# Kernel tuning notes

Measured on AMD Instinct MI355X. Metric: run time of the kernel, lower is better.

Reference implementation:

```python
import jax, jax.numpy as jnp
import numpy as np

HEADS = 4

def _layernorm(x, g, b, eps=1e-5):
    mu = x.mean(-1, keepdims=True)
    var = ((x - mu) ** 2).mean(-1, keepdims=True)
    return (x - mu) / jnp.sqrt(var + eps) * g + b

def _feature_map(data, proj, is_query, eps=1e-4):
    # FAVOR+ softmax kernel features. data: [B,H,S,dh], proj: [m,dh]
    dh = data.shape[-1]
    m = proj.shape[0]
    dn = dh ** -0.25
    ratio = m ** -0.5
    dash = jnp.einsum('bhsd,md->bhsm', data * dn, proj)
    diag = 0.5 * jnp.sum((data * dn) ** 2, axis=-1, keepdims=True)
    mx = jnp.max(dash, axis=-1, keepdims=True) if is_query else jnp.max(dash)
    return ratio * (jnp.exp(dash - diag - mx) + eps)

def _causal_linear_attention(q, k, v):
    # q,k: [B,H,S,m] kernel features; v: [B,H,S,dh]
    k_cum = jnp.cumsum(k, axis=2)                                  # [B,H,S,m]
    d_inv = 1.0 / jnp.einsum('bhsm,bhsm->bhs', q, k_cum)           # [B,H,S]
    ctx = jnp.cumsum(jnp.einsum('bhsm,bhsd->bhsmd', k, v), axis=2) # [B,H,S,m,dh]
    return jnp.einsum('bhsmd,bhsm,bhs->bhsd', ctx, q, d_inv)

def reference(x, pre_w, pre_b, ln1_g, ln1_b, wq, wk, wv, wo, bo, proj,
              ln2_g, ln2_b, ff_w1, ff_b1, ff_w2, ff_b2, tgt_w, tgt_b, rd_w, rd_b):
    # preproc: 1x1x1 conv3d + softplus
    xbn = jax.nn.softplus(jnp.einsum('bcthw,oc->bothw', x, pre_w)
                          + pre_b[None, :, None, None, None])
    B, D, T, H, W = xbn.shape
    tokens = xbn.reshape(B, -1, D)  # raw torch-style reshape, S = T*H*W
    S = tokens.shape[1]

    # Performer block (depth=1): prenorm attention + prenorm FF, residuals
    h = _layernorm(tokens, ln1_g, ln1_b)
    split = lambda t: t.reshape(B, S, HEADS, -1).transpose(0, 2, 1, 3)
    q, k, v = split(h @ wq), split(h @ wk), split(h @ wv)
    qp = _feature_map(q, proj, True)
    kp = _feature_map(k, proj, False)
    attn = _causal_linear_attention(qp, kp, v)
    attn = attn.transpose(0, 2, 1, 3).reshape(B, S, D)
    tokens = tokens + attn @ wo + bo
    h2 = _layernorm(tokens, ln2_g, ln2_b)
    tokens = tokens + jax.nn.gelu(h2 @ ff_w1 + ff_b1, approximate=False) @ ff_w2 + ff_b2

    # readout
    out = tokens.reshape(B, D, T, H, W).mean(axis=2)               # [B,D,H,W]
    out = jnp.concatenate([out, x[:, 2, 0][:, None]], axis=1)      # [B,D+1,H,W]
    out = jax.lax.conv_general_dilated(out, tgt_w, (1, 1), [(2, 2), (2, 2)],
                                       dimension_numbers=('NCHW', 'OIHW', 'NCHW'))
    out = out + tgt_b[None, :, None, None]
    out = out.mean(axis=(2, 3))                                    # global avg pool -> [B,1]
    return out @ rd_w.T + rd_b


def setup_inputs() -> dict:
    key = jax.random.key(0)
    ks = jax.random.split(key, 12)
    B, T, H, W = 2, 8, 48, 48
    D, DH, M, FF = 64, 16, 32, 256
    s = lambda k, shape, sc=1.0: jax.random.normal(k, shape, jnp.float32) * sc
    inv = 1.0 / np.sqrt(D)
    return {
        'x': s(ks[0], (B, 3, T, H, W)),
        'pre_w': s(ks[1], (D, 3), 1.0 / np.sqrt(3)),
        'pre_b': jnp.zeros((D,), jnp.float32),
        'ln1_g': jnp.ones((D,), jnp.float32), 'ln1_b': jnp.zeros((D,), jnp.float32),
        'wq': s(ks[2], (D, D), inv), 'wk': s(ks[3], (D, D), inv), 'wv': s(ks[4], (D, D), inv),
        'wo': s(ks[5], (D, D), inv), 'bo': jnp.zeros((D,), jnp.float32),
        'proj': s(ks[6], (M, DH)),
        'ln2_g': jnp.ones((D,), jnp.float32), 'ln2_b': jnp.zeros((D,), jnp.float32),
        'ff_w1': s(ks[7], (D, FF), inv), 'ff_b1': jnp.zeros((FF,), jnp.float32),
        'ff_w2': s(ks[8], (FF, D), 1.0 / np.sqrt(FF)), 'ff_b2': jnp.zeros((D,), jnp.float32),
        'tgt_w': s(ks[9], (1, D + 1, 5, 5), 1.0 / np.sqrt((D + 1) * 25)),
        'tgt_b': jnp.zeros((1,), jnp.float32),
        'rd_w': s(ks[10], (1, 1)), 'rd_b': jnp.zeros((1,), jnp.float32),
    }
```

## Files before the change

### kernel.cpp

```cpp
#include <hip/hip_runtime.h>
#include <hip/hip_bf16.h>
#include <math.h>

typedef __hip_bfloat16 bf16;
typedef __attribute__((ext_vector_type(8))) short short8;
typedef __attribute__((ext_vector_type(16))) float floatx16;

constexpr int B_   = 2;
constexpr int T_   = 8;
constexpr int HW   = 48 * 48;
constexpr int S_   = T_ * HW;
constexpr int D_   = 64;
constexpr int NH   = 4;
constexpr int DH   = 16;
constexpr int M_   = 32;
constexpr int BS   = B_ * S_;
constexpr int BSD  = BS * D_;
constexpr int BH   = B_ * NH;
constexpr int BHS  = BH * S_;
constexpr int BHSM = BHS * M_;
constexpr int CHUNK = 32;
constexpr int NC   = S_ / CHUNK;
constexpr int STATE = M_ * DH + M_;
constexpr float DN = 0.5f;
constexpr float RATIO = 0.17677669529663687f;

__device__ __forceinline__ unsigned short f2bf(float f) {
  bf16 h = __float2bfloat16(f);
  return *reinterpret_cast<unsigned short*>(&h);
}
__device__ __forceinline__ float bf2f(bf16 v) { return __bfloat162float(v); }

__global__ void k_preln(const float* __restrict__ x, const float* __restrict__ pw,
                        const float* __restrict__ pb, const float* __restrict__ g,
                        const float* __restrict__ bb,
                        float* __restrict__ tok, bf16* __restrict__ h) {
  int token = blockIdx.x * 4 + (threadIdx.x >> 6);
  int lane = threadIdx.x & 63;
  int f = token * 64 + lane;
  int b = f / (D_ * S_);
  int r = f % (D_ * S_);
  int d = r / S_;
  int pos = r % S_;
  const float* xb = x + b * 3 * S_ + pos;
  float a = xb[0] * pw[d * 3 + 0] + xb[S_] * pw[d * 3 + 1] + xb[2 * S_] * pw[d * 3 + 2]
          + pb[d];
  float t = fmaxf(a, 0.f) + log1pf(expf(-fabsf(a)));
  tok[f] = t;
  float s1 = t, s2 = t * t;
  for (int off = 32; off; off >>= 1) {
    s1 += __shfl_xor(s1, off);
    s2 += __shfl_xor(s2, off);
  }
  float mu = s1 * (1.f / 64.f);
  float var = s2 * (1.f / 64.f) - mu * mu;
  float rs = rsqrtf(var + 1e-5f);
  h[f] = __float2bfloat16((t - mu) * rs * g[lane] + bb[lane]);
}

__global__ void __launch_bounds__(192) k_qkv(const bf16* __restrict__ h,
                      const float* __restrict__ wq, const float* __restrict__ wk,
                      const float* __restrict__ wv,
                      bf16* __restrict__ q, bf16* __restrict__ k, bf16* __restrict__ v) {
  int tid = threadIdx.x;
  int w = tid >> 6;
  int L = tid & 63;
  int half = L >> 5;
  int n = L & 31;
  int tbase = blockIdx.x * 32;
  const float* wm = (w == 0) ? wq : (w == 1) ? wk : wv;
  bf16* outm = (w == 0) ? q : (w == 1) ? k : v;

  short8 a[4];
  {
    const bf16* hrow = h + (size_t)(tbase + n) * 64 + half * 8;
#pragma unroll
    for (int c = 0; c < 4; ++c) a[c] = *(const short8*)(hrow + c * 16);
  }
#pragma unroll
  for (int ct = 0; ct < 2; ++ct) {
    int col = ct * 32 + n;
    short8 bfrag[4];
#pragma unroll
    for (int c = 0; c < 4; ++c) {
#pragma unroll
      for (int j = 0; j < 8; ++j)
        bfrag[c][j] = (short)f2bf(wm[(c * 16 + half * 8 + j) * 64 + col]);
    }
    floatx16 acc;
#pragma unroll
    for (int i = 0; i < 16; ++i) acc[i] = 0.f;
    acc = __builtin_amdgcn_mfma_f32_32x32x16_bf16(a[0], bfrag[0], acc, 0, 0, 0);
    acc = __builtin_amdgcn_mfma_f32_32x32x16_bf16(a[1], bfrag[1], acc, 0, 0, 0);
    acc = __builtin_amdgcn_mfma_f32_32x32x16_bf16(a[2], bfrag[2], acc, 0, 0, 0);
    acc = __builtin_amdgcn_mfma_f32_32x32x16_bf16(a[3], bfrag[3], acc, 0, 0, 0);
    int head = col >> 4, di = col & 15;
#pragma unroll
    for (int r = 0; r < 16; ++r) {
      int row = (r & 3) + 8 * (r >> 2) + 4 * half;
      int token = tbase + row;
      int b = token / S_, s = token % S_;
      outm[((size_t)(b * NH + head) * S_ + s) * DH + di] = __float2bfloat16(acc[r]);
    }
  }
}

__global__ void __launch_bounds__(256) k_feat(const bf16* __restrict__ q,
                      const bf16* __restrict__ k, const float* __restrict__ proj,
                      bf16* __restrict__ qpb, float* __restrict__ kp,
                      float* __restrict__ diagk, float* __restrict__ part) {
  int tid = threadIdx.x;
  int w = tid >> 6;
  int L = tid & 63;
  int half = L >> 5;
  int n = L & 31;
  int rowbase = blockIdx.x * 128 + w * 32;

  short8 qs = *(const short8*)(q + (size_t)(rowbase + n) * 16 + half * 8);
  short8 ks = *(const short8*)(k + (size_t)(rowbase + n) * 16 + half * 8);
  short8 aq, ak, bp;
  float dq = 0.f, dk = 0.f;
#pragma unroll
  for (int j = 0; j < 8; ++j) {
    float qf = __uint_as_float(((unsigned)(unsigned short)qs[j]) << 16) * DN;
    float kf = __uint_as_float(((unsigned)(unsigned short)ks[j]) << 16) * DN;
    dq += qf * qf; dk += kf * kf;
    aq[j] = (short)f2bf(qf);
    ak[j] = (short)f2bf(kf);
    bp[j] = (short)f2bf(proj[n * 16 + half * 8 + j]);
  }
  dq += __shfl_xor(dq, 32);
  dk += __shfl_xor(dk, 32);
  dq *= 0.5f; dk *= 0.5f;

  floatx16 Pq, Pk;
#pragma unroll
  for (int i = 0; i < 16; ++i) { Pq[i] = 0.f; Pk[i] = 0.f; }
  Pq = __builtin_amdgcn_mfma_f32_32x32x16_bf16(aq, bp, Pq, 0, 0, 0);
  Pk = __builtin_amdgcn_mfma_f32_32x32x16_bf16(ak, bp, Pk, 0, 0, 0);

  float bmax = -3.4e38f;
#pragma unroll
  for (int r = 0; r < 16; ++r) {
    int i = (r & 3) + 8 * (r >> 2) + 4 * half;
    kp[(size_t)(rowbase + i) * 32 + n] = Pk[r];
    bmax = fmaxf(bmax, Pk[r]);
  }
  if (L < 32) diagk[rowbase + n] = dk;
  for (int off = 32; off; off >>= 1) bmax = fmaxf(bmax, __shfl_xor(bmax, off));
  if (L == 0) part[blockIdx.x * 4 + w] = bmax;

#pragma unroll
  for (int r = 0; r < 16; ++r) {
    int i = (r & 3) + 8 * (r >> 2) + 4 * half;
    float mx = Pq[r];
    for (int off = 16; off; off >>= 1) mx = fmaxf(mx, __shfl_xor(mx, off, 32));
    float dqi = __shfl(dq, i, 64);
    float val = RATIO * (expf(Pq[r] - dqi - mx) + 1e-4f);
    qpb[(size_t)(rowbase + i) * 32 + n] = __float2bfloat16(val);
  }
}

__global__ void k_maxred(const float* __restrict__ part, float* __restrict__ gmax) {
  float m = -3.4e38f;
  for (int i = threadIdx.x; i < BHS / 32; i += 256) m = fmaxf(m, part[i]);
  __shared__ float red[256];
  red[threadIdx.x] = m;
  __syncthreads();
  for (int s = 128; s; s >>= 1) {
    if (threadIdx.x < s) red[threadIdx.x] = fmaxf(red[threadIdx.x], red[threadIdx.x + s]);
    __syncthreads();
  }
  if (!threadIdx.x) gmax[0] = red[0];
}

__global__ void __launch_bounds__(256) k_csfin(const float* __restrict__ diagk,
                      const float* __restrict__ gmax, const bf16* __restrict__ v,
                      const float* __restrict__ kp, bf16* __restrict__ kpb,
                      float* __restrict__ ckv) {
  __shared__ __align__(16) float sKp[CHUNK * 32];
  __shared__ __align__(16) float sVc[CHUNK * 16];
  int blk = blockIdx.x;
  int bh = blk / NC, c = blk % NC;
  int tid = threadIdx.x;
  int base = bh * S_ + c * CHUNK;
  float gm = gmax[0];
  {
    int row = tid >> 3, m4 = tid & 7;
    float4 dash = *(const float4*)&kp[(size_t)(base + row) * 32 + m4 * 4];
    float dg = diagk[base + row] + gm;
    float4 fin;
    fin.x = RATIO * (expf(dash.x - dg) + 1e-4f);
    fin.y = RATIO * (expf(dash.y - dg) + 1e-4f);
    fin.z = RATIO * (expf(dash.z - dg) + 1e-4f);
    fin.w = RATIO * (expf(dash.w - dg) + 1e-4f);
    *(float4*)&sKp[row * 32 + m4 * 4] = fin;
    uint2 u;
    u.x = (unsigned)f2bf(fin.x) | ((unsigned)f2bf(fin.y) << 16);
    u.y = (unsigned)f2bf(fin.z) | ((unsigned)f2bf(fin.w) << 16);
    *(uint2*)&kpb[(size_t)(base + row) * 32 + m4 * 4] = u;
  }
  if (tid < 128) {
    int row = tid >> 2, c4 = tid & 3;
    const bf16* vr = v + (size_t)(base + row) * 16 + c4 * 4;
    sVc[row * 16 + c4 * 4 + 0] = bf2f(vr[0]);
    sVc[row * 16 + c4 * 4 + 1] = bf2f(vr[1]);
    sVc[row * 16 + c4 * 4 + 2] = bf2f(vr[2]);
    sVc[row * 16 + c4 * 4 + 3] = bf2f(vr[3]);
  }
  __syncthreads();
  int m0 = tid >> 4, d0 = tid & 15;
  int m1 = m0 + 16;
  float a0 = 0.f, a1 = 0.f, az0 = 0.f, az1 = 0.f;
  for (int t = 0; t < CHUNK; ++t) {
    float k0 = sKp[t * 32 + m0];
    float k1 = sKp[t * 32 + m1];
    float vv = sVc[t * 16 + d0];
    a0 += k0 * vv;
    a1 += k1 * vv;
    if (d0 == 0) { az0 += k0; az1 += k1; }
  }
  float* outp = ckv + (size_t)blk * STATE;
  outp[m0 * 16 + d0] = a0;
  outp[m1 * 16 + d0] = a1;
  if (d0 == 0) { outp[512 + m0] = az0; outp[512 + m1] = az1; }
}

__global__ void k_prefix(float* __restrict__ ckv) {
  int idx = blockIdx.x * 256 + threadIdx.x;
  int bh = idx / STATE, c = idx % STATE;
  float run = 0.f;
  for (int j0 = 0; j0 < NC; j0 += 16) {
    float tb[16];
#pragma unroll
    for (int jj = 0; jj < 16; ++jj) tb[jj] = ckv[((size_t)bh * NC + j0 + jj) * STATE + c];
#pragma unroll
    for (int jj = 0; jj < 16; ++jj) {
      ckv[((size_t)bh * NC + j0 + jj) * STATE + c] = run;
      run += tb[jj];
    }
  }
}

__global__ void __launch_bounds__(256) k_attn(const bf16* __restrict__ qpb,
                                              const bf16* __restrict__ kpb,
                                              const bf16* __restrict__ v,
                                              const float* __restrict__ ckv,
                                              bf16* __restrict__ attn) {
  __shared__ __align__(16) float sP[4][32 * 33 + 4];
  int tid = threadIdx.x;
  int w = tid >> 6;
  int L = tid & 63;
  int half = L >> 5;
  int n = L & 31;
  int chunk = blockIdx.x * 4 + w;
  int bh = chunk / NC, c = chunk % NC;
  int base = bh * S_ + c * CHUNK;

  short8 a1 = *(const short8*)(qpb + (size_t)(base + n) * 32 + half * 8);
  short8 a2 = *(const short8*)(qpb + (size_t)(base + n) * 32 + 16 + half * 8);
  short8 b1 = *(const short8*)(kpb + (size_t)(base + n) * 32 + half * 8);
  short8 b2 = *(const short8*)(kpb + (size_t)(base + n) * 32 + 16 + half * 8);

  floatx16 P;
#pragma unroll
  for (int i = 0; i < 16; ++i) P[i] = 0.f;
  P = __builtin_amdgcn_mfma_f32_32x32x16_bf16(a1, b1, P, 0, 0, 0);
  P = __builtin_amdgcn_mfma_f32_32x32x16_bf16(a2, b2, P, 0, 0, 0);

  float* sp = &sP[w][0];
#pragma unroll
  for (int r = 0; r < 16; ++r) {
    int i = (r & 3) + 8 * (r >> 2) + 4 * half;
    sp[i * 33 + n] = (n <= i) ? P[r] : 0.f;
  }
  __syncthreads();
  short8 pa1, pa2;
#pragma unroll
  for (int j = 0; j < 8; ++j) {
    pa1[j] = (short)f2bf(sp[n * 33 + half * 8 + j]);
    pa2[j] = (short)f2bf(sp[n * 33 + 16 + half * 8 + j]);
  }

  const float* cs = ckv + (size_t)chunk * STATE;
  const unsigned short one_bf = f2bf(1.f);
  short8 vb1, vb2, sb1, sb2;
#pragma unroll
  for (int j = 0; j < 8; ++j) {
    int t1 = half * 8 + j, t2 = 16 + half * 8 + j;
    vb1[j] = (n < 16) ? *(const short*)(v + (size_t)(base + t1) * 16 + n)
                      : (short)(n == 16 ? one_bf : 0);
    vb2[j] = (n < 16) ? *(const short*)(v + (size_t)(base + t2) * 16 + n)
                      : (short)(n == 16 ? one_bf : 0);
    float y1 = (n < 16) ? cs[t1 * 16 + n] : (n == 16 ? cs[512 + t1] : 0.f);
    float y2 = (n < 16) ? cs[t2 * 16 + n] : (n == 16 ? cs[512 + t2] : 0.f);
    sb1[j] = (short)f2bf(y1);
    sb2[j] = (short)f2bf(y2);
  }

  floatx16 O;
#pragma unroll
  for (int i = 0; i < 16; ++i) O[i] = 0.f;
  O = __builtin_amdgcn_mfma_f32_32x32x16_bf16(pa1, vb1, O, 0, 0, 0);
  O = __builtin_amdgcn_mfma_f32_32x32x16_bf16(pa2, vb2, O, 0, 0, 0);
  O = __builtin_amdgcn_mfma_f32_32x32x16_bf16(a1, sb1, O, 0, 0, 0);
  O = __builtin_amdgcn_mfma_f32_32x32x16_bf16(a2, sb2, O, 0, 0, 0);

  int srcl = 16 + 32 * half;
  float res[16];
#pragma unroll
  for (int r = 0; r < 16; ++r) {
    float den = __shfl(O[r], srcl, 64);
    res[r] = O[r] / den;
  }
  if (n < 16) {
    int b = bh >> 2, head = bh & 3;
#pragma unroll
    for (int r = 0; r < 16; ++r) {
      int i = (r & 3) + 8 * (r >> 2) + 4 * half;
      attn[((size_t)(b * S_ + c * CHUNK + i)) * 64 + head * 16 + n] = __float2bfloat16(res[r]);
    }
  }
}

__global__ void __launch_bounds__(128) k_wo_ln(const bf16* __restrict__ attn,
                        const float* __restrict__ wo, const float* __restrict__ bo,
                        const float* __restrict__ tok, const float* __restrict__ g,
                        const float* __restrict__ bb,
                        float* __restrict__ tok2, bf16* __restrict__ h2) {
  __shared__ __align__(16) float sC[32 * 68];
  int tid = threadIdx.x;
  int w = tid >> 6;
  int L = tid & 63;
  int half = L >> 5;
  int n = L & 31;
  int tbase = blockIdx.x * 32;

  short8 a[4];
  {
    const bf16* arow = attn + (size_t)(tbase + n) * 64 + half * 8;
#pragma unroll
    for (int c = 0; c < 4; ++c) a[c] = *(const short8*)(arow + c * 16);
  }
  int col = w * 32 + n;
  short8 bfrag[4];
#pragma unroll
  for (int c = 0; c < 4; ++c) {
#pragma unroll
    for (int j = 0; j < 8; ++j)
      bfrag[c][j] = (short)f2bf(wo[(c * 16 + half * 8 + j) * 64 + col]);
  }
  floatx16 acc;
#pragma unroll
  for (int i = 0; i < 16; ++i) acc[i] = 0.f;
  acc = __builtin_amdgcn_mfma_f32_32x32x16_bf16(a[0], bfrag[0], acc, 0, 0, 0);
  acc = __builtin_amdgcn_mfma_f32_32x32x16_bf16(a[1], bfrag[1], acc, 0, 0, 0);
  acc = __builtin_amdgcn_mfma_f32_32x32x16_bf16(a[2], bfrag[2], acc, 0, 0, 0);
  acc = __builtin_amdgcn_mfma_f32_32x32x16_bf16(a[3], bfrag[3], acc, 0, 0, 0);
  float bias = bo[col];
#pragma unroll
  for (int r = 0; r < 16; ++r) {
    int row = (r & 3) + 8 * (r >> 2) + 4 * half;
    sC[row * 68 + col] = acc[r] + tok[(size_t)(tbase + row) * 64 + col] + bias;
  }
  __syncthreads();
  int tg = tid >> 5, cg = tid & 31;
  int c0 = cg * 2, c1 = c0 + 1;
  float g0 = g[c0], g1 = g[c1], be0 = bb[c0], be1 = bb[c1];
#pragma unroll
  for (int i = 0; i < 8; ++i) {
    int lrow = tg * 8 + i;
    int token = tbase + lrow;
    float t0 = sC[lrow * 68 + c0];
    float t1 = sC[lrow * 68 + c1];
    float s1 = t0 + t1, s2 = t0 * t0 + t1 * t1;
    for (int off = 16; off; off >>= 1) {
      s1 += __shfl_xor(s1, off, 32);
      s2 += __shfl_xor(s2, off, 32);
    }
    float mu = s1 * (1.f / 64.f);
    float var = s2 * (1.f / 64.f) - mu * mu;
    float rs = rsqrtf(var + 1e-5f);
    tok2[token * 64 + c0] = t0;
    tok2[token * 64 + c1] = t1;
    h2[token * 64 + c0] = __float2bfloat16((t0 - mu) * rs * g0 + be0);
    h2[token * 64 + c1] = __float2bfloat16((t1 - mu) * rs * g1 + be1);
  }
}

__global__ void __launch_bounds__(256) k_ffg(const bf16* __restrict__ h2,
                                             const float* __restrict__ w1,
                                             const float* __restrict__ b1,
                                             float* __restrict__ Gavg) {
  int tid = threadIdx.x;
  int w = tid >> 6;
  int L = tid & 63;
  int half = L >> 5;
  int n = L & 31;
  int blk = blockIdx.x;
  int b = blk / 576;
  int rem = blk % 576;
  int ch = rem / 9;
  int jp0 = (rem % 9) * 4;
  int token_n = b * 18432 + ch * 288 + (n & 7) * 36 + jp0 + (n >> 3);

  short8 a[4];
  {
    const bf16* hrow = h2 + (size_t)token_n * 64 + half * 8;
#pragma unroll
    for (int c = 0; c < 4; ++c) a[c] = *(const short8*)(hrow + c * 16);
  }
  size_t gbase = ((size_t)(b * 64 + ch) * 36 + jp0);
#pragma unroll
  for (int ct = 0; ct < 2; ++ct) {
    int col = w * 64 + ct * 32 + n;
    short8 bfrag[4];
#pragma unroll
    for (int c = 0; c < 4; ++c) {
#pragma unroll
      for (int j = 0; j < 8; ++j)
        bfrag[c][j] = (short)f2bf(w1[(c * 16 + half * 8 + j) * 256 + col]);
    }
    floatx16 acc;
#pragma unroll
    for (int i = 0; i < 16; ++i) acc[i] = 0.f;
    acc = __builtin_amdgcn_mfma_f32_32x32x16_bf16(a[0], bfrag[0], acc, 0, 0, 0);
    acc = __builtin_amdgcn_mfma_f32_32x32x16_bf16(a[1], bfrag[1], acc, 0, 0, 0);
    acc = __builtin_amdgcn_mfma_f32_32x32x16_bf16(a[2], bfrag[2], acc, 0, 0, 0);
    acc = __builtin_amdgcn_mfma_f32_32x32x16_bf16(a[3], bfrag[3], acc, 0, 0, 0);
    float bias = b1[col];
#pragma unroll
    for (int j = 0; j < 4; ++j) {
      float s = 0.f;
#pragma unroll
      for (int rr = 0; rr < 4; ++rr) {
        float xg = acc[j * 4 + rr] + bias;
        s += 0.5f * xg * (1.f + erff(xg * 0.70710678118654752f));
      }
      s += __shfl_xor(s, 32);
      if (half == 0)
        Gavg[(gbase + j) * 256 + col] = s * 0.125f;
    }
  }
}

__global__ void __launch_bounds__(256) k_pool2(const float* __restrict__ Gavg,
                        const float* __restrict__ tok2, const float* __restrict__ w2,
                        const float* __restrict__ b2, float* __restrict__ pool) {
  __shared__ __align__(16) float sG[18 * 256];
  __shared__ __align__(16) float sRed[4 * 18 * 64];
  int blk = blockIdx.x;
  int b = blk / 128;
  int rem = blk % 128;
  int ch = rem >> 1, jph = rem & 1;
  int tid = threadIdx.x;
  size_t grow0 = ((size_t)(b * 64 + ch) * 36 + jph * 18) * 256;
  for (int e = tid; e < 1152; e += 256) {
    int row = e >> 6, c4 = e & 63;
    *(float4*)&sG[row * 256 + c4 * 4] = *(const float4*)&Gavg[grow0 + row * 256 + c4 * 4];
  }
  __syncthreads();
  int kg = tid >> 6, dd = tid & 63;
  float acc[18];
#pragma unroll
  for (int i = 0; i < 18; ++i) acc[i] = 0.f;
  for (int k4 = 0; k4 < 16; ++k4) {
    int k = kg * 64 + k4 * 4;
    float w0 = w2[(k + 0) * 64 + dd];
    float w1 = w2[(k + 1) * 64 + dd];
    float w2v = w2[(k + 2) * 64 + dd];
    float w3 = w2[(k + 3) * 64 + dd];
#pragma unroll
    for (int i = 0; i < 18; ++i) {
      float4 gf = *(const float4*)&sG[i * 256 + k];
      acc[i] += gf.x * w0 + gf.y * w1 + gf.z * w2v + gf.w * w3;
    }
  }
#pragma unroll
  for (int i = 0; i < 18; ++i) sRed[(kg * 18 + i) * 64 + dd] = acc[i];
  __syncthreads();
  for (int o = tid; o < 1152; o += 256) {
    int jp18 = o >> 6, d2 = o & 63;
    float gsum = sRed[(0 * 18 + jp18) * 64 + d2] + sRed[(1 * 18 + jp18) * 64 + d2]
               + sRed[(2 * 18 + jp18) * 64 + d2] + sRed[(3 * 18 + jp18) * 64 + d2];
    int p = (jph * 18 + jp18) * 64 + d2;
    size_t tbase = (size_t)b * 1179648 + (size_t)ch * 18432 + p;
    float ts = 0.f;
#pragma unroll
    for (int t = 0; t < 8; ++t) ts += tok2[tbase + t * 2304];
    pool[((size_t)(b * 64 + ch)) * HW + p] = ts * 0.125f + gsum + b2[d2];
  }
}

__global__ void __launch_bounds__(256) k_convsum(const float* __restrict__ pool,
                                                 const float* __restrict__ x,
                                                 const float* __restrict__ w,
                                                 float* __restrict__ partial) {
  int blk = blockIdx.x;
  int b = blk / 65, ch = blk % 65;
  int tid = threadIdx.x;
  __shared__ float cls[25];
  __shared__ float red[256];
  if (tid < 25) {
    int ry = tid / 5, rx = tid % 5;
    int kh0 = (ry <= 2) ? 0 : (ry == 3 ? 1 : 2);
    int kh1 = (ry >= 2) ? 4 : (ry == 1 ? 3 : 2);
    int kw0 = (rx <= 2) ? 0 : (rx == 3 ? 1 : 2);
    int kw1 = (rx >= 2) ? 4 : (rx == 1 ? 3 : 2);
    float s = 0.f;
    for (int kh = kh0; kh <= kh1; ++kh)
      for (int kw = kw0; kw <= kw1; ++kw)
        s += w[ch * 25 + kh * 5 + kw];
    cls[tid] = s;
  }
  __syncthreads();
  const float* pc = (ch < 64) ? (pool + ((size_t)(b * 64 + ch)) * HW)
                              : (x + (size_t)b * 3 * S_ + 2 * S_);
  float acc = 0.f;
#pragma unroll
  for (int e = tid; e < HW; e += 256) {
    int iy = e / 48, ix = e % 48;
    int ry = (iy == 0) ? 0 : (iy == 1) ? 1 : (iy <= 45) ? 2 : (iy == 46) ? 3 : 4;
    int rx = (ix == 0) ? 0 : (ix == 1) ? 1 : (ix <= 45) ? 2 : (ix == 46) ? 3 : 4;
    acc += pc[e] * cls[ry * 5 + rx];
  }
  red[tid] = acc;
  __syncthreads();
  for (int s = 128; s; s >>= 1) {
    if (tid < s) red[tid] += red[tid + s];
    __syncthreads();
  }
  if (!tid) partial[blk] = red[0];
}

__global__ void k_final(const float* __restrict__ partial, const float* __restrict__ tgt_b,
                        const float* __restrict__ rd_w, const float* __restrict__ rd_b,
                        float* __restrict__ out) {
  int b = blockIdx.x;
  int lane = threadIdx.x;
  float s = (lane < 65) ? partial[b * 65 + lane] : 0.f;
  for (int off = 32; off; off >>= 1) s += __shfl_down(s, off, 64);
  __shared__ float r2;
  if (lane == 64) r2 = s;
  __syncthreads();
  if (!lane) {
    float tot = s + r2;
    float mean = tot / 2304.f + tgt_b[0];
    out[b] = mean * rd_w[0] + rd_b[0];
  }
}

extern "C" void kernel_launch(void* const* d_in, const int* in_sizes, int n_in,
                              void* d_out, int out_size, void* d_ws, size_t ws_size,
                              hipStream_t stream) {
  const float* x     = (const float*)d_in[0];
  const float* pre_w = (const float*)d_in[1];
  const float* pre_b = (const float*)d_in[2];
  const float* ln1_g = (const float*)d_in[3];
  const float* ln1_b = (const float*)d_in[4];
  const float* wq    = (const float*)d_in[5];
  const float* wk    = (const float*)d_in[6];
  const float* wv    = (const float*)d_in[7];
  const float* wo    = (const float*)d_in[8];
  const float* bo    = (const float*)d_in[9];
  const float* proj  = (const float*)d_in[10];
  const float* ln2_g = (const float*)d_in[11];
  const float* ln2_b = (const float*)d_in[12];
  const float* ff_w1 = (const float*)d_in[13];
  const float* ff_b1 = (const float*)d_in[14];
  const float* ff_w2 = (const float*)d_in[15];
  const float* ff_b2 = (const float*)d_in[16];
  const float* tgt_w = (const float*)d_in[17];
  const float* tgt_b = (const float*)d_in[18];
  const float* rd_w  = (const float*)d_in[19];
  const float* rd_b  = (const float*)d_in[20];
  float* out = (float*)d_out;

  float* ws = (float*)d_ws;
  float* tok   = ws;
  bf16*  v     = (bf16*)(ws + (size_t)BSD);
  bf16*  q     = (bf16*)(ws + 2 * (size_t)BSD);
  float* Gavg  = ws + 2 * (size_t)BSD;
  float* pool  = Gavg + 1179648;
  bf16*  k     = (bf16*)(ws + 3 * (size_t)BSD);
  bf16*  h     = (bf16*)(ws + 4 * (size_t)BSD);
  float* kp    = ws + 4 * (size_t)BSD;
  bf16*  qpb   = (bf16*)(ws + 6 * (size_t)BSD);
  bf16*  kpb   = (bf16*)(ws + 7 * (size_t)BSD);
  float* ckv   = ws + 8 * (size_t)BSD;
  float* tok2  = ws + 8 * (size_t)BSD;
  bf16*  attnb = k;
  bf16*  h2    = h;
  float* smalls = ws + 9 * (size_t)BSD + 147456;
  float* diagk = smalls;
  float* part  = diagk + BHS;
  float* gmax  = part + BHSM / 256;
  float* partial = gmax + 64;

  k_preln<<<dim3(BS / 4), dim3(256), 0, stream>>>(x, pre_w, pre_b, ln1_g, ln1_b, tok, h);
  k_qkv<<<dim3(BS / 32), dim3(192), 0, stream>>>(h, wq, wk, wv, q, k, v);
  k_feat<<<dim3(BHS / 128), dim3(256), 0, stream>>>(q, k, proj, qpb, kp, diagk, part);
  k_maxred<<<dim3(1), dim3(256), 0, stream>>>(part, gmax);
  k_csfin<<<dim3(BH * NC), dim3(256), 0, stream>>>(diagk, gmax, v, kp, kpb, ckv);
  k_prefix<<<dim3(BH * STATE / 256), dim3(256), 0, stream>>>(ckv);
  k_attn<<<dim3(BH * NC / 4), dim3(256), 0, stream>>>(qpb, kpb, v, ckv, attnb);
  k_wo_ln<<<dim3(BS / 32), dim3(128), 0, stream>>>(attnb, wo, bo, tok, ln2_g, ln2_b, tok2, h2);
  k_ffg<<<dim3(B_ * 64 * 9), dim3(256), 0, stream>>>(h2, ff_w1, ff_b1, Gavg);
  k_pool2<<<dim3(B_ * 64 * 2), dim3(256), 0, stream>>>(Gavg, tok2, ff_w2, ff_b2, pool);
  k_convsum<<<dim3(B_ * 65), dim3(256), 0, stream>>>(pool, x, tgt_w, partial);
  k_final<<<dim3(B_), dim3(128), 0, stream>>>(partial, tgt_b, rd_w, rd_b, out);
}
```

Measured before the change: 222.9 us.

## Split chunk-state prefix scan into three-phase segmented scan; store residual tokens as bf16

The single serial prefix-sum kernel over 576 chunks per head is replaced by a three-phase segmented scan: per-segment sums, a scan over the 18 segment sums, then a per-segment rescan seeded with its offset. This raises parallelism from BH*STATE threads to 18 times that, so the former long serial dependency chain is spread over many more waves. Separately, the residual token buffers tok and tok2 are stored as bf16 instead of fp32 to halve their memory traffic. The cost is two extra launches, an extra read of the chunk states, and reduced precision on the residual stream.

```diff
diff --git a/kernel.cpp b/kernel.cpp
--- a/kernel.cpp
+++ b/kernel.cpp
@@ -21,6 +21,8 @@
 constexpr int BHSM = BHS * M_;
 constexpr int CHUNK = 32;
 constexpr int NC   = S_ / CHUNK;
+constexpr int NSEG = 18;
+constexpr int SEGLEN = 32;
 constexpr int STATE = M_ * DH + M_;
 constexpr float DN = 0.5f;
 constexpr float RATIO = 0.17677669529663687f;
@@ -34,7 +36,7 @@
 __global__ void k_preln(const float* __restrict__ x, const float* __restrict__ pw,
                         const float* __restrict__ pb, const float* __restrict__ g,
                         const float* __restrict__ bb,
-                        float* __restrict__ tok, bf16* __restrict__ h) {
+                        bf16* __restrict__ tok, bf16* __restrict__ h) {
   int token = blockIdx.x * 4 + (threadIdx.x >> 6);
   int lane = threadIdx.x & 63;
   int f = token * 64 + lane;
@@ -46,7 +48,7 @@
   float a = xb[0] * pw[d * 3 + 0] + xb[S_] * pw[d * 3 + 1] + xb[2 * S_] * pw[d * 3 + 2]
           + pb[d];
   float t = fmaxf(a, 0.f) + log1pf(expf(-fabsf(a)));
-  tok[f] = t;
+  tok[f] = __float2bfloat16(t);
   float s1 = t, s2 = t * t;
   for (int off = 32; off; off >>= 1) {
     s1 += __shfl_xor(s1, off);
@@ -226,18 +228,51 @@
   if (d0 == 0) { outp[512 + m0] = az0; outp[512 + m1] = az1; }
 }
 
-__global__ void k_prefix(float* __restrict__ ckv) {
+__global__ void k_scan1(const float* __restrict__ ckv, float* __restrict__ segsum) {
   int idx = blockIdx.x * 256 + threadIdx.x;
-  int bh = idx / STATE, c = idx % STATE;
+  int c = idx % STATE;
+  int rem = idx / STATE;
+  int seg = rem % NSEG;
+  int bh = rem / NSEG;
+  size_t base = ((size_t)bh * NC + seg * SEGLEN) * STATE + c;
+  float s = 0.f;
+#pragma unroll 8
+  for (int i = 0; i < SEGLEN; ++i) s += ckv[base + (size_t)i * STATE];
+  segsum[idx] = s;
+}
+
+__global__ void k_scan2(float* __restrict__ segsum) {
+  int idx = blockIdx.x * 256 + threadIdx.x;
+  int c = idx % STATE;
+  int bh = idx / STATE;
+  float tb[NSEG];
+#pragma unroll
+  for (int s = 0; s < NSEG; ++s)
+    tb[s] = segsum[((size_t)bh * NSEG + s) * STATE + c];
   float run = 0.f;
-  for (int j0 = 0; j0 < NC; j0 += 16) {
-    float tb[16];
-#pragma unroll
-    for (int jj = 0; jj < 16; ++jj) tb[jj] = ckv[((size_t)bh * NC + j0 + jj) * STATE + c];
-#pragma unroll
-    for (int jj = 0; jj < 16; ++jj) {
-      ckv[((size_t)bh * NC + j0 + jj) * STATE + c] = run;
-      run += tb[jj];
+#pragma unroll
+  for (int s = 0; s < NSEG; ++s) {
+    segsum[((size_t)bh * NSEG + s) * STATE + c] = run;
+    run += tb[s];
+  }
+}
+
+__global__ void k_scan3(float* __restrict__ ckv, const float* __restrict__ segsum) {
+  int idx = blockIdx.x * 256 + threadIdx.x;
+  int c = idx % STATE;
+  int rem = idx / STATE;
+  int seg = rem % NSEG;
+  int bh = rem / NSEG;
+  float run = segsum[idx];
+  size_t base = ((size_t)bh * NC + seg * SEGLEN) * STATE + c;
+  for (int i0 = 0; i0 < SEGLEN; i0 += 8) {
+    float tb[8];
+#pragma unroll
+    for (int j = 0; j < 8; ++j) tb[j] = ckv[base + (size_t)(i0 + j) * STATE];
+#pragma unroll
+    for (int j = 0; j < 8; ++j) {
+      ckv[base + (size_t)(i0 + j) * STATE] = run;
+      run += tb[j];
     }
   }
 }
@@ -325,9 +360,9 @@
 
 __global__ void __launch_bounds__(128) k_wo_ln(const bf16* __restrict__ attn,
                         const float* __restrict__ wo, const float* __restrict__ bo,
-                        const float* __restrict__ tok, const float* __restrict__ g,
+                        const bf16* __restrict__ tok, const float* __restrict__ g,
                         const float* __restrict__ bb,
-                        float* __restrict__ tok2, bf16* __restrict__ h2) {
+                        bf16* __restrict__ tok2, bf16* __restrict__ h2) {
   __shared__ __align__(16) float sC[32 * 68];
   int tid = threadIdx.x;
   int w = tid >> 6;
@@ -361,7 +396,7 @@
 #pragma unroll
   for (int r = 0; r < 16; ++r) {
     int row = (r & 3) + 8 * (r >> 2) + 4 * half;
-    sC[row * 68 + col] = acc[r] + tok[(size_t)(tbase + row) * 64 + col] + bias;
+    sC[row * 68 + col] = acc[r] + bf2f(tok[(size_t)(tbase + row) * 64 + col]) + bias;
   }
   __syncthreads();
   int tg = tid >> 5, cg = tid & 31;
@@ -381,8 +416,8 @@
     float mu = s1 * (1.f / 64.f);
     float var = s2 * (1.f / 64.f) - mu * mu;
     float rs = rsqrtf(var + 1e-5f);
-    tok2[token * 64 + c0] = t0;
-    tok2[token * 64 + c1] = t1;
+    tok2[token * 64 + c0] = __float2bfloat16(t0);
+    tok2[token * 64 + c1] = __float2bfloat16(t1);
     h2[token * 64 + c0] = __float2bfloat16((t0 - mu) * rs * g0 + be0);
     h2[token * 64 + c1] = __float2bfloat16((t1 - mu) * rs * g1 + be1);
   }
@@ -445,7 +480,7 @@
 }
 
 __global__ void __launch_bounds__(256) k_pool2(const float* __restrict__ Gavg,
-                        const float* __restrict__ tok2, const float* __restrict__ w2,
+                        const bf16* __restrict__ tok2, const float* __restrict__ w2,
                         const float* __restrict__ b2, float* __restrict__ pool) {
   __shared__ __align__(16) float sG[18 * 256];
   __shared__ __align__(16) float sRed[4 * 18 * 64];
@@ -487,7 +522,7 @@
     size_t tbase = (size_t)b * 1179648 + (size_t)ch * 18432 + p;
     float ts = 0.f;
 #pragma unroll
-    for (int t = 0; t < 8; ++t) ts += tok2[tbase + t * 2304];
+    for (int t = 0; t < 8; ++t) ts += bf2f(tok2[tbase + t * 2304]);
     pool[((size_t)(b * 64 + ch)) * HW + p] = ts * 0.125f + gsum + b2[d2];
   }
 }
@@ -577,7 +612,7 @@
   float* out = (float*)d_out;
 
   float* ws = (float*)d_ws;
-  float* tok   = ws;
+  bf16*  tok   = (bf16*)ws;
   bf16*  v     = (bf16*)(ws + (size_t)BSD);
   bf16*  q     = (bf16*)(ws + 2 * (size_t)BSD);
   float* Gavg  = ws + 2 * (size_t)BSD;
@@ -588,7 +623,7 @@
   bf16*  qpb   = (bf16*)(ws + 6 * (size_t)BSD);
   bf16*  kpb   = (bf16*)(ws + 7 * (size_t)BSD);
   float* ckv   = ws + 8 * (size_t)BSD;
-  float* tok2  = ws + 8 * (size_t)BSD;
+  bf16*  tok2  = (bf16*)(ws + 8 * (size_t)BSD);
   bf16*  attnb = k;
   bf16*  h2    = h;
   float* smalls = ws + 9 * (size_t)BSD + 147456;
@@ -596,13 +631,16 @@
   float* part  = diagk + BHS;
   float* gmax  = part + BHSM / 256;
   float* partial = gmax + 64;
+  float* segsum  = partial + 256;
 
   k_preln<<<dim3(BS / 4), dim3(256), 0, stream>>>(x, pre_w, pre_b, ln1_g, ln1_b, tok, h);
   k_qkv<<<dim3(BS / 32), dim3(192), 0, stream>>>(h, wq, wk, wv, q, k, v);
   k_feat<<<dim3(BHS / 128), dim3(256), 0, stream>>>(q, k, proj, qpb, kp, diagk, part);
   k_maxred<<<dim3(1), dim3(256), 0, stream>>>(part, gmax);
   k_csfin<<<dim3(BH * NC), dim3(256), 0, stream>>>(diagk, gmax, v, kp, kpb, ckv);
-  k_prefix<<<dim3(BH * STATE / 256), dim3(256), 0, stream>>>(ckv);
+  k_scan1<<<dim3(BH * NSEG * STATE / 256), dim3(256), 0, stream>>>(ckv, segsum);
+  k_scan2<<<dim3(BH * STATE / 256), dim3(256), 0, stream>>>(segsum);
+  k_scan3<<<dim3(BH * NSEG * STATE / 256), dim3(256), 0, stream>>>(ckv, segsum);
   k_attn<<<dim3(BH * NC / 4), dim3(256), 0, stream>>>(qpb, kpb, v, ckv, attnb);
   k_wo_ln<<<dim3(BS / 32), dim3(128), 0, stream>>>(attnb, wo, bo, tok, ln2_g, ln2_b, tok2, h2);
   k_ffg<<<dim3(B_ * 64 * 9), dim3(256), 0, stream>>>(h2, ff_w1, ff_b1, Gavg);
```

After: 212.6 us (median of 2 runs). -4.6%, faster.
